# Kernel tuning notes

Hardware: AMD Instinct MI355X
Metric: run time of the kernel (lower is better)

Reference implementation:

```python
import jax, jax.numpy as jnp
import numpy as np

B, C_IN, C_OUT = 8, 64, 64
H, W = 256, 256
FH, FW = 16, 16  # patch grid from weight map spatial dims
HYPER_PARAMS = C_OUT * C_IN  # kernel_size=1, groups=1


def setup_inputs() -> dict:
    key = jax.random.key(0)
    kx, ks = jax.random.split(key)
    x = jax.random.normal(kx, (B, C_IN, H, W), dtype=jnp.float32)
    # s is the hypernetwork-generated per-patch weight map [b, out*in, fh, fw]
    s = jax.random.normal(ks, (B, HYPER_PARAMS, FH, FW), dtype=jnp.float32)
    return {"x": x, "s": s}


def reference(x, s):
    b, c, h, w = x.shape
    fh, fw = s.shape[-2], s.shape[-1]
    ph, pw = h // fh, w // fw
    out_ch = s.shape[1] // c  # hyper_params = out_ch * c (1x1 kernel, groups=1)
    # weight.permute(0,2,3,1).reshape(b*fh*fw*out, in, 1, 1) -> per-patch [out, in]
    Wp = jnp.transpose(s, (0, 2, 3, 1)).reshape(b, fh, fw, out_ch, c)
    # x.view(b,c,fh,ph,fw,pw).permute(0,2,4,1,3,5) -> per-patch blocks [b,fh,fw,c,ph,pw]
    xp = jnp.transpose(x.reshape(b, c, fh, ph, fw, pw), (0, 2, 4, 1, 3, 5))
    # grouped 1x1 conv over b*fh*fw groups == batched small matmul per patch
    y = jnp.einsum('bijoc,bijcpq->bijopq', Wp, xp)
    # .view(b,fh,fw,-1,ph,pw).permute(0,3,1,4,2,5).reshape(b,-1,h,w)
    return jnp.transpose(y, (0, 3, 1, 4, 2, 5)).reshape(b, out_ch, h, w)
```

## Files before the change

kernel.cpp:

```cpp
#include <hip/hip_runtime.h>

#define NB 8
#define FH 16
#define FW 16

typedef __bf16 bf16x8 __attribute__((ext_vector_type(8)));
typedef float  f32x4  __attribute__((ext_vector_type(4)));

#define WS_BYTES ((size_t)NB * 256 * 512 * 16)

__global__ __launch_bounds__(256) void pack_w_kernel(
    const float* __restrict__ s, bf16x8* __restrict__ ws)
{
    __shared__ float lds[16 * 513];
    const int bid = blockIdx.x;
    const int b   = bid & 7;
    const int kk  = (bid >> 3) & 1;
    const int mt  = (bid >> 4) & 3;
    const int pi  = (bid >> 6) & 15;
    const int tid = threadIdx.x;

    #pragma unroll
    for (int pass = 0; pass < 8; ++pass) {
        const int idx   = pass * 256 + tid;
        const int u     = idx >> 2;
        const int pj4   = idx & 3;
        const int row16 = u >> 5;
        const int cc    = u & 31;
        const size_t row = (size_t)b * 4096 + mt * 1024 + row16 * 64 + kk * 32 + cc;
        const float4 v = *reinterpret_cast<const float4*>(
            s + row * 256 + pi * 16 + pj4 * 4);
        lds[(pj4 * 4 + 0) * 513 + cc * 16 + row16] = v.x;
        lds[(pj4 * 4 + 1) * 513 + cc * 16 + row16] = v.y;
        lds[(pj4 * 4 + 2) * 513 + cc * 16 + row16] = v.z;
        lds[(pj4 * 4 + 3) * 513 + cc * 16 + row16] = v.w;
    }
    __syncthreads();

    const int gl     = tid & 63;
    const int row16  = gl & 15;
    const int lanehi = gl >> 4;
    #pragma unroll
    for (int pjblk = 0; pjblk < 4; ++pjblk) {
        const int pj = pjblk * 4 + (tid >> 6);
        bf16x8 e;
        #pragma unroll
        for (int j = 0; j < 8; ++j)
            e[j] = (__bf16)lds[pj * 513 + (lanehi * 8 + j) * 16 + row16];
        ws[((size_t)(b * 256 + pi * 16 + pj)) * 512 + (mt * 2 + kk) * 64 + gl] = e;
    }
}

__global__ __launch_bounds__(256, 3) void gemm_kernel(
    const float* __restrict__ x,
    const bf16x8* __restrict__ ws,
    float* __restrict__ out)
{
    __shared__ char smem[32768];
    float* smemf = (float*)smem;

    const int bid = blockIdx.x;
    const int b   = bid & 7;
    const int h   = bid >> 3;
    const int pi  = h >> 4;
    const int t   = threadIdx.x;
    const int lane = t & 63;
    const int wv   = t >> 6;
    const int q    = lane & 15;
    const int hi   = lane >> 4;

    {
        const float* xrow = x + (size_t)b * 64 * 65536 + (size_t)h * 256;
        #pragma unroll
        for (int oo = 0; oo < 2; ++oo) {
            const int co = wv * 2 + oo;
            f32x4 v[8];
            #pragma unroll
            for (int cc = 0; cc < 8; ++cc)
                v[cc] = *(const f32x4*)(xrow + (size_t)(co * 8 + cc) * 65536
                                        + lane * 4);
            #pragma unroll
            for (int i = 0; i < 4; ++i) {
                const int w = lane * 4 + i;
                bf16x8 e;
                #pragma unroll
                for (int cc = 0; cc < 8; ++cc)
                    e[cc] = (__bf16)v[cc][i];
                *(bf16x8*)(smem + w * 128 + ((co ^ (w & 7)) * 16)) = e;
            }
        }
    }
    __syncthreads();

    f32x4 acc[4][4];
    #pragma unroll
    for (int j = 0; j < 4; ++j) {
        const int pj = wv * 4 + j;
        const bf16x8* wbase = ws + ((size_t)(b * 256 + pi * 16 + pj)) * 512;
        bf16x8 bf[2];
        #pragma unroll
        for (int kk = 0; kk < 2; ++kk) {
            const int w  = pj * 16 + q;
            const int co = kk * 4 + hi;
            bf[kk] = *(const bf16x8*)(smem + w * 128 + ((co ^ (w & 7)) * 16));
        }
        #pragma unroll
        for (int mt = 0; mt < 4; ++mt) {
            acc[j][mt] = (f32x4){0.f, 0.f, 0.f, 0.f};
            acc[j][mt] = __builtin_amdgcn_mfma_f32_16x16x32_bf16(
                wbase[(mt * 2 + 0) * 64 + lane], bf[0], acc[j][mt], 0, 0, 0);
            acc[j][mt] = __builtin_amdgcn_mfma_f32_16x16x32_bf16(
                wbase[(mt * 2 + 1) * 64 + lane], bf[1], acc[j][mt], 0, 0, 0);
        }
        __builtin_amdgcn_sched_barrier(0);
    }
    __syncthreads();

    #pragma unroll
    for (int h2 = 0; h2 < 2; ++h2) {
        #pragma unroll
        for (int j = 0; j < 4; ++j) {
            const int w = (wv * 4 + j) * 16 + q;
            #pragma unroll
            for (int m2 = 0; m2 < 2; ++m2) {
                const int mt = h2 * 2 + m2;
                #pragma unroll
                for (int r = 0; r < 4; ++r) {
                    const int o2 = m2 * 16 + hi * 4 + r;
                    smemf[o2 * 256 + (w ^ ((o2 & 7) << 2))] = acc[j][mt][r];
                }
            }
        }
        __syncthreads();

        #pragma unroll
        for (int ps = 0; ps < 8; ++ps) {
            const int o2 = ps * 4 + wv;
            f32x4 vv = *(const f32x4*)&smemf[o2 * 256
                                             + ((lane * 4) ^ ((o2 & 7) << 2))];
            *(f32x4*)(out + (size_t)(b * 64 + h2 * 32 + o2) * 65536
                          + (size_t)h * 256 + lane * 4) = vv;
        }
        if (h2 == 0) __syncthreads();
    }
}

__global__ __launch_bounds__(512) void hyperpatch_fallback(
    const float* __restrict__ x,
    const float* __restrict__ s,
    float* __restrict__ out)
{
    __shared__ bf16x8 afrag[2][512];
    const int bid = blockIdx.x;
    const int b   = bid >> 7;
    const int pi  = (bid >> 3) & 15;
    const int pj0 = (bid & 7) * 2;
    const int t   = threadIdx.x;
    const int lane = t & 63;
    const int wv   = t >> 6;

    {
        const int g  = t;
        const int mt = g >> 7;
        const int kk = (g >> 6) & 1;
        const int gl = g & 63;
        const int o  = mt * 16 + (gl & 15);
        const int c0 = kk * 32 + (gl >> 4) * 8;
        const float2* sb2 = reinterpret_cast<const float2*>(
            s + ((size_t)b * 4096) * 256 + pi * 16 + pj0);
        bf16x8 ta, tb;
        #pragma unroll
        for (int j = 0; j < 8; ++j) {
            float2 v = sb2[(size_t)(o * 64 + c0 + j) * 128];
            ta[j] = (__bf16)v.x;
            tb[j] = (__bf16)v.y;
        }
        afrag[0][g] = ta;
        afrag[1][g] = tb;
    }

    const int pat  = wv >> 2;
    const int wrow = wv & 3;
    const int q  = lane & 15;
    const int cb = (lane >> 4) * 8;
    const float* xbase = x + (((size_t)b * 64) * 256 + pi * 16) * 256
                           + (pj0 + pat) * 16 + q;
    bf16x8 bfrag[4][2];
    #pragma unroll
    for (int nt = 0; nt < 4; ++nt) {
        const int p = wrow * 4 + nt;
        #pragma unroll
        for (int kk = 0; kk < 2; ++kk) {
            const int c = kk * 32 + cb;
            bf16x8 tv;
            #pragma unroll
            for (int j = 0; j < 8; ++j) {
                float v = xbase[(size_t)(c + j) * 65536 + (size_t)p * 256];
                tv[j] = (__bf16)v;
            }
            bfrag[nt][kk] = tv;
        }
    }

    __syncthreads();

    bf16x8 a[4][2];
    #pragma unroll
    for (int mt = 0; mt < 4; ++mt)
        #pragma unroll
        for (int kk = 0; kk < 2; ++kk)
            a[mt][kk] = afrag[pat][(mt * 2 + kk) * 64 + lane];

    f32x4 acc[4][4];
    #pragma unroll
    for (int mt = 0; mt < 4; ++mt)
        #pragma unroll
        for (int nt = 0; nt < 4; ++nt)
            acc[mt][nt] = (f32x4){0.f, 0.f, 0.f, 0.f};

    #pragma unroll
    for (int mt = 0; mt < 4; ++mt) {
        #pragma unroll
        for (int nt = 0; nt < 4; ++nt) {
            acc[mt][nt] = __builtin_amdgcn_mfma_f32_16x16x32_bf16(
                a[mt][0], bfrag[nt][0], acc[mt][nt], 0, 0, 0);
            acc[mt][nt] = __builtin_amdgcn_mfma_f32_16x16x32_bf16(
                a[mt][1], bfrag[nt][1], acc[mt][nt], 0, 0, 0);
        }
    }

    const int ro = (lane >> 4) * 4;
    float* obase = out + (((size_t)b * 64) * 256 + pi * 16) * 256
                       + (pj0 + pat) * 16 + q;
    #pragma unroll
    for (int mt = 0; mt < 4; ++mt) {
        #pragma unroll
        for (int nt = 0; nt < 4; ++nt) {
            const int p = wrow * 4 + nt;
            #pragma unroll
            for (int r = 0; r < 4; ++r) {
                const int o = mt * 16 + ro + r;
                obase[(size_t)o * 65536 + (size_t)p * 256] = acc[mt][nt][r];
            }
        }
    }
}

extern "C" void kernel_launch(void* const* d_in, const int* in_sizes, int n_in,
                              void* d_out, int out_size, void* d_ws, size_t ws_size,
                              hipStream_t stream)
{
    (void)in_sizes; (void)n_in; (void)out_size;
    const float* x = (const float*)d_in[0];
    const float* s = (const float*)d_in[1];
    float* out = (float*)d_out;

    if (ws_size >= WS_BYTES && d_ws != nullptr) {
        bf16x8* ws = (bf16x8*)d_ws;
        pack_w_kernel<<<dim3(1024), dim3(256), 0, stream>>>(s, ws);
        gemm_kernel<<<dim3(2048), dim3(256), 0, stream>>>(x, ws, out);
    } else {
        hyperpatch_fallback<<<dim3(NB * FH * (FW / 2)), dim3(512), 0, stream>>>(x, s, out);
    }
}
```

Measured before the change: 80.84 us.

## Load x tile directly into LDS as fp32 and convert to bf16 at fragment read

The x row tile is now brought into LDS with global_load_lds direct-to-LDS transfers in fp32, instead of going through registers and being converted and transposed into a swizzled bf16 layout. The B fragments are built by reading eight scalar fp32 values per fragment from LDS and converting them on the fly. LDS use doubles to 64KB, the occupancy hint of 3 blocks and the sched_barrier are removed. This cuts register traffic and conversion work in the load phase, at the cost of more scalar LDS reads (with possible bank conflicts) and lower occupancy from the larger LDS footprint.

```diff
diff --git a/kernel.cpp b/kernel.cpp
--- a/kernel.cpp
+++ b/kernel.cpp
@@ -51,14 +51,12 @@
     }
 }
 
-__global__ __launch_bounds__(256, 3) void gemm_kernel(
+__global__ __launch_bounds__(256) void gemm_kernel(
     const float* __restrict__ x,
     const bf16x8* __restrict__ ws,
     float* __restrict__ out)
 {
-    __shared__ char smem[32768];
-    float* smemf = (float*)smem;
-
+    __shared__ float smemf[16384];
     const int bid = blockIdx.x;
     const int b   = bid & 7;
     const int h   = bid >> 3;
@@ -70,39 +68,35 @@
     const int hi   = lane >> 4;
 
     {
-        const float* xrow = x + (size_t)b * 64 * 65536 + (size_t)h * 256;
-        #pragma unroll
-        for (int oo = 0; oo < 2; ++oo) {
-            const int co = wv * 2 + oo;
-            f32x4 v[8];
-            #pragma unroll
-            for (int cc = 0; cc < 8; ++cc)
-                v[cc] = *(const f32x4*)(xrow + (size_t)(co * 8 + cc) * 65536
-                                        + lane * 4);
-            #pragma unroll
-            for (int i = 0; i < 4; ++i) {
-                const int w = lane * 4 + i;
-                bf16x8 e;
-                #pragma unroll
-                for (int cc = 0; cc < 8; ++cc)
-                    e[cc] = (__bf16)v[cc][i];
-                *(bf16x8*)(smem + w * 128 + ((co ^ (w & 7)) * 16)) = e;
-            }
-        }
-    }
+        const float* xrow = x + (size_t)b * 64 * 65536 + (size_t)h * 256 + lane * 4;
+        #pragma unroll
+        for (int k = 0; k < 16; ++k) {
+            const int c = wv * 16 + k;
+            __builtin_amdgcn_global_load_lds(
+                (const __attribute__((address_space(1))) void*)(xrow + (size_t)c * 65536),
+                (__attribute__((address_space(3))) void*)(&smemf[c * 256]),
+                16, 0, 0);
+        }
+    }
+    asm volatile("s_waitcnt vmcnt(0)" ::: "memory");
     __syncthreads();
 
     f32x4 acc[4][4];
     #pragma unroll
     for (int j = 0; j < 4; ++j) {
         const int pj = wv * 4 + j;
+        const int w  = pj * 16 + q;
         const bf16x8* wbase = ws + ((size_t)(b * 256 + pi * 16 + pj)) * 512;
         bf16x8 bf[2];
         #pragma unroll
         for (int kk = 0; kk < 2; ++kk) {
-            const int w  = pj * 16 + q;
-            const int co = kk * 4 + hi;
-            bf[kk] = *(const bf16x8*)(smem + w * 128 + ((co ^ (w & 7)) * 16));
+            bf16x8 e;
+            #pragma unroll
+            for (int jj = 0; jj < 8; ++jj) {
+                const int c = kk * 32 + hi * 8 + jj;
+                e[jj] = (__bf16)smemf[c * 256 + w];
+            }
+            bf[kk] = e;
         }
         #pragma unroll
         for (int mt = 0; mt < 4; ++mt) {
@@ -112,7 +106,6 @@
             acc[j][mt] = __builtin_amdgcn_mfma_f32_16x16x32_bf16(
                 wbase[(mt * 2 + 1) * 64 + lane], bf[1], acc[j][mt], 0, 0, 0);
         }
-        __builtin_amdgcn_sched_barrier(0);
     }
     __syncthreads();
 
```

New measurement: 89.07 us. 1.1x slower.
